# Performance work log

Hardware: AMD Instinct MI355X
Metric: run time of the kernel (lower is better)

Reference implementation:

```python
import jax, jax.numpy as jnp
import numpy as np
import math

B, L, D, H, DK, DV = 4, 1024, 1024, 16, 64, 64


def setup_inputs() -> dict:
    key0 = jax.random.key(0)
    ks = jax.random.split(key0, 12)
    s = 0.02
    return {
        "key":   jax.random.normal(ks[0], (B, L, D), jnp.float32),
        "value": jax.random.normal(ks[1], (B, L, D), jnp.float32),
        "query": jax.random.normal(ks[2], (B, L, D), jnp.float32),
        "mask":  jax.random.randint(ks[3], (B, L, L), 0, 2).astype(bool),
        "Wq": jax.random.normal(ks[4], (D, H * DK), jnp.float32) * s,
        "bq": jnp.zeros((H * DK,), jnp.float32),
        "Wk": jax.random.normal(ks[5], (D, H * DK), jnp.float32) * s,
        "bk": jnp.zeros((H * DK,), jnp.float32),
        "Wv": jax.random.normal(ks[6], (D, H * DV), jnp.float32) * s,
        "bv": jnp.zeros((H * DV,), jnp.float32),
        "Wo": jax.random.normal(ks[7], (H * DV, D), jnp.float32) * s,
        "bo": jnp.zeros((D,), jnp.float32),
    }


def _shape(x, d):
    # (B, L, H*d) -> (B, H, L, d)
    b, l, _ = x.shape
    return x.reshape(b, l, H, d).transpose(0, 2, 1, 3)


def reference(key, value, query, mask, Wq, bq, Wk, bk, Wv, bv, Wo, bo):
    k = _shape(key @ Wk + bk, DK)       # (B,H,L,DK)
    v = _shape(value @ Wv + bv, DV)     # (B,H,L,DV)
    q = _shape(query @ Wq + bq, DK) / math.sqrt(DK)
    scores = jnp.einsum("bhqd,bhkd->bhqk", q, k)  # (B,H,L,L) fp32
    scores = jnp.where(mask[:, None, :, :], jnp.float32(-1e18), scores)
    # coverage (training path, step=None): triangular cumulative penalty
    maxes = jnp.max(scores, axis=3, keepdims=True)
    exp_score = jnp.exp(scores - maxes)
    # tril-ones matmul over exp_score[:, :, :-1, :] == cumsum along query axis
    penalty_body = jnp.cumsum(exp_score[:, :, :-1, :], axis=2)
    no_penalty = jnp.ones_like(penalty_body[:, :, :1, :])
    penalty = jnp.concatenate([no_penalty, penalty_body], axis=2)
    unnorm = exp_score / (penalty + 1e-8)
    attn = unnorm / jnp.sum(unnorm, axis=3, keepdims=True)
    context = jnp.einsum("bhqk,bhkd->bhqd", attn, v)  # (B,H,L,DV)
    context = context.transpose(0, 2, 1, 3).reshape(B, L, H * DV)
    final_output = context @ Wo + bo  # (B,L,D)
    return final_output
```

## Files before the change

kernel.cpp:

```cpp
#include <hip/hip_runtime.h>
#include <hip/hip_bf16.h>


typedef unsigned short u16;
typedef unsigned int u32;
typedef __bf16 v8bf __attribute__((ext_vector_type(8)));
typedef u16    v8us __attribute__((ext_vector_type(8)));
typedef float  v4f  __attribute__((ext_vector_type(4)));

__device__ __forceinline__ u16 f2b(float f){
  __hip_bfloat16 h = __float2bfloat16(f);
  return __builtin_bit_cast(u16, h);
}

__global__ void detect_kernel(const u32* __restrict__ m, int* __restrict__ flag){
  __shared__ int sb1, sb3, snz;
  int tid = threadIdx.x;
  if (tid == 0){ sb1 = 0; sb3 = 0; snz = 0; }
  __syncthreads();
  int l1 = 0, l3 = 0, ln = 0;
  for (int i = tid; i < 65536; i += 256){
    u32 v = m[i];
    u32 b1 = (v >> 8) & 0xffu, b2 = (v >> 16) & 0xffu, b3 = (v >> 24) & 0xffu;
    l1 |= (b1 == 0x3fu);
    l3 |= (b3 == 0x3fu);
    ln |= ((b1 | b2 | b3) != 0u);
  }
  if (l1) atomicOr(&sb1, 1);
  if (l3) atomicOr(&sb3, 1);
  if (ln) atomicOr(&snz, 1);
  __syncthreads();
  if (tid == 0) *flag = sb1 ? 3 : (sb3 ? 2 : (snz ? 0 : 1));
}

__global__ __launch_bounds__(256)
void pack_mask(const void* __restrict__ m, const int* __restrict__ modep,
               u32* __restrict__ bm)
{
  const int w = blockIdx.x * 256 + threadIdx.x;
  const int mode = *modep;
  u32 out = 0;
  if (mode == 0){
    const u32* p = (const u32*)m + (size_t)w * 8;
    #pragma unroll
    for (int i = 0; i < 8; i++){
      u32 v = p[i];
      if (v & 0x000000ffu) out |= 1u << (4*i+0);
      if (v & 0x0000ff00u) out |= 1u << (4*i+1);
      if (v & 0x00ff0000u) out |= 1u << (4*i+2);
      if (v & 0xff000000u) out |= 1u << (4*i+3);
    }
  } else if (mode == 3){
    const u16* p = (const u16*)m + (size_t)w * 32;
    for (int i = 0; i < 32; i++) if (p[i]) out |= 1u << i;
  } else {
    const u32* p = (const u32*)m + (size_t)w * 32;
    for (int i = 0; i < 32; i++) if (p[i]) out |= 1u << i;
  }
  bm[w] = out;
}

__global__ __launch_bounds__(256)
void cast_bf16(const float* __restrict__ in, u16* __restrict__ out){
  const int i = blockIdx.x * 256 + threadIdx.x;
  const float4* p = (const float4*)(in + (size_t)i * 8);
  float4 a = p[0], b = p[1];
  v8us r;
  r[0]=f2b(a.x); r[1]=f2b(a.y); r[2]=f2b(a.z); r[3]=f2b(a.w);
  r[4]=f2b(b.x); r[5]=f2b(b.y); r[6]=f2b(b.z); r[7]=f2b(b.w);
  ((v8us*)out)[i] = r;
}

__global__ __launch_bounds__(256)
void transpose_cast(const float* __restrict__ W, u16* __restrict__ Wt){
  __shared__ float T[64][65];
  const int ki = blockIdx.y, ni = blockIdx.x, t = threadIdx.x;
  const int r = t >> 2, c4 = (t & 3) * 16;
  const float4* src = (const float4*)&W[(size_t)(ki*64 + r) * 1024 + ni*64 + c4];
  #pragma unroll
  for (int i = 0; i < 4; i++){
    float4 f = src[i];
    T[r][c4+4*i+0]=f.x; T[r][c4+4*i+1]=f.y; T[r][c4+4*i+2]=f.z; T[r][c4+4*i+3]=f.w;
  }
  __syncthreads();
  u16* dst = &Wt[(size_t)(ni*64 + r) * 1024 + ki*64 + c4];
  v8us o0, o1;
  #pragma unroll
  for (int j = 0; j < 8; j++){ o0[j] = f2b(T[c4+j][r]); o1[j] = f2b(T[c4+8+j][r]); }
  *(v8us*)dst = o0;
  *(v8us*)(dst + 8) = o1;
}

template<int OMODE>
__global__ __launch_bounds__(256)
void gemm_gl(const u16* __restrict__ A, const u16* __restrict__ Wt,
             const float* __restrict__ bias, float scale, void* __restrict__ outp)
{
  __shared__ alignas(16) u16 As[128 * 64];
  __shared__ alignas(16) u16 Bs[64 * 64];
  const int tid = threadIdx.x, l = tid & 63, w = tid >> 6;
  const int li = l & 15, g = l >> 4;
  const int rowBase = blockIdx.y * 128, colBase = blockIdx.x * 64;
  const int wm = w >> 1, wn = w & 1;

  v4f acc[4][2];
  #pragma unroll
  for (int i = 0; i < 4; i++)
    #pragma unroll
    for (int j = 0; j < 2; j++) acc[i][j] = (v4f){0.f,0.f,0.f,0.f};

  for (int kt = 0; kt < 16; ++kt){
    const int k0 = kt * 64;
    __syncthreads();
    #pragma unroll
    for (int j = 0; j < 4; ++j){
      const int s = j * 256 + tid;
      const int r = s >> 3, c8 = s & 7;
      const int c8s = c8 ^ (r & 7);
      const u16* src = &A[(size_t)(rowBase + r) * 1024 + k0 + c8s * 8];
      __builtin_amdgcn_global_load_lds(
        (const __attribute__((address_space(1))) void*)src,
        (__attribute__((address_space(3))) void*)(As + (size_t)(j*256 + w*64) * 8),
        16, 0, 0);
    }
    #pragma unroll
    for (int j = 0; j < 2; ++j){
      const int s = j * 256 + tid;
      const int r = s >> 3, c8 = s & 7;
      const int c8s = c8 ^ (r & 7);
      const u16* src = &Wt[(size_t)(colBase + r) * 1024 + k0 + c8s * 8];
      __builtin_amdgcn_global_load_lds(
        (const __attribute__((address_space(1))) void*)src,
        (__attribute__((address_space(3))) void*)(Bs + (size_t)(j*256 + w*64) * 8),
        16, 0, 0);
    }
    __syncthreads();
    #pragma unroll
    for (int kk = 0; kk < 2; ++kk){
      v8bf af[4], bf[2];
      #pragma unroll
      for (int mt = 0; mt < 4; ++mt){
        const int r = wm*64 + mt*16 + li;
        af[mt] = *(const v8bf*)&As[r*64 + (((kk*4 + g) ^ (r & 7)) * 8)];
      }
      #pragma unroll
      for (int nt = 0; nt < 2; ++nt){
        const int c = wn*32 + nt*16 + li;
        bf[nt] = *(const v8bf*)&Bs[c*64 + (((kk*4 + g) ^ (c & 7)) * 8)];
      }
      #pragma unroll
      for (int mt = 0; mt < 4; ++mt)
        #pragma unroll
        for (int nt = 0; nt < 2; ++nt)
          acc[mt][nt] = __builtin_amdgcn_mfma_f32_16x16x32_bf16(af[mt], bf[nt], acc[mt][nt], 0, 0, 0);
    }
  }

  #pragma unroll
  for (int mt = 0; mt < 4; ++mt){
    #pragma unroll
    for (int nt = 0; nt < 2; ++nt){
      const int gc = colBase + wn*32 + nt*16 + li;
      const float bs = bias[gc];
      #pragma unroll
      for (int r = 0; r < 4; ++r){
        const int gr = rowBase + wm*64 + mt*16 + g*4 + r;
        float v = acc[mt][nt][r] + bs;
        if (OMODE == 0){
          v *= scale;
          const int bb = gr >> 10, lp = gr & 1023;
          const int h = gc >> 6, dk = gc & 63;
          ((u16*)outp)[((((size_t)bb*16 + h) << 10) + lp) * 64 + dk] = f2b(v);
        } else {
          ((float*)outp)[(size_t)gr * 1024 + gc] = v;
        }
      }
    }
  }
}

__global__ __launch_bounds__(256)
void rowmax_kernel(const u16* __restrict__ Qb, const u16* __restrict__ Kb,
                   const u32* __restrict__ bm, float* __restrict__ mbuf)
{
  const int tid = threadIdx.x, l = tid & 63, w = tid >> 6;
  const int li = l & 15, g = l >> 4;
  const int bid = blockIdx.x;
  const int bh = bid >> 4, qb = bid & 15;
  const int b = bh >> 4;
  const int qrow0 = qb * 64 + w * 16;
  const u32* bmb = bm + ((size_t)b << 15);

  const u16* qbase = &Qb[((size_t)bh * 1024 + qrow0 + li) * 64 + g * 8];
  const v8bf a0 = *(const v8bf*)qbase;
  const v8bf a1 = *(const v8bf*)(qbase + 32);

  float rm[4] = {-3.0e38f, -3.0e38f, -3.0e38f, -3.0e38f};

  for (int kt = 0; kt < 64; ++kt){
    const u16* kbase = &Kb[((size_t)bh * 1024 + kt*16 + li) * 64 + g * 8];
    v8bf b0 = *(const v8bf*)kbase;
    v8bf b1 = *(const v8bf*)(kbase + 32);
    v4f s = (v4f){0.f,0.f,0.f,0.f};
    s = __builtin_amdgcn_mfma_f32_16x16x32_bf16(a0, b0, s, 0, 0, 0);
    s = __builtin_amdgcn_mfma_f32_16x16x32_bf16(a1, b1, s, 0, 0, 0);
    const int bit = ((kt & 1) << 4) + li;
    #pragma unroll
    for (int r = 0; r < 4; ++r){
      const int row = qrow0 + g*4 + r;
      const u32 mw = bmb[(row << 5) | (kt >> 1)];
      const float sv = ((mw >> bit) & 1u) ? -1e18f : s[r];
      rm[r] = fmaxf(rm[r], sv);
    }
  }
  #pragma unroll
  for (int r = 0; r < 4; ++r){
    float v = rm[r];
    v = fmaxf(v, __shfl_xor(v, 1));
    v = fmaxf(v, __shfl_xor(v, 2));
    v = fmaxf(v, __shfl_xor(v, 4));
    v = fmaxf(v, __shfl_xor(v, 8));
    rm[r] = v;
  }
  if (li == 0){
    #pragma unroll
    for (int r = 0; r < 4; ++r)
      mbuf[(size_t)bh * 1024 + qrow0 + g*4 + r] = rm[r];
  }
}

__global__ __launch_bounds__(256)
void colsum_kernel(const u16* __restrict__ Qb, const u16* __restrict__ Kb,
                   const u32* __restrict__ bm, const float* __restrict__ mbuf,
                   float* __restrict__ Tsum)
{
  __shared__ float Tw[4][256];
  const int tid = threadIdx.x, l = tid & 63, w = tid >> 6;
  const int li = l & 15, g = l >> 4;
  const int bid = blockIdx.x;
  const int bh = bid >> 6, qc = (bid >> 2) & 15, kb = bid & 3;
  const int b = bh >> 4;
  const int col0 = kb * 256;
  const int qrow0 = qc * 64 + w * 16;
  const u32* bmb = bm + ((size_t)b << 15);

  const u16* qbase = &Qb[((size_t)bh * 1024 + qrow0 + li) * 64 + g * 8];
  const v8bf a0 = *(const v8bf*)qbase;
  const v8bf a1 = *(const v8bf*)(qbase + 32);
  float mrow[4];
  #pragma unroll
  for (int r = 0; r < 4; ++r) mrow[r] = mbuf[(size_t)bh * 1024 + qrow0 + g*4 + r];

  #pragma unroll
  for (int nt = 0; nt < 16; ++nt){
    const u16* kbase = &Kb[((size_t)bh * 1024 + col0 + nt*16 + li) * 64 + g * 8];
    v8bf b0 = *(const v8bf*)kbase;
    v8bf b1 = *(const v8bf*)(kbase + 32);
    v4f s = (v4f){0.f,0.f,0.f,0.f};
    s = __builtin_amdgcn_mfma_f32_16x16x32_bf16(a0, b0, s, 0, 0, 0);
    s = __builtin_amdgcn_mfma_f32_16x16x32_bf16(a1, b1, s, 0, 0, 0);
    const int wi = (col0 >> 5) + (nt >> 1);
    const int bit = ((nt & 1) << 4) + li;
    float t = 0.f;
    #pragma unroll
    for (int r = 0; r < 4; ++r){
      const int row = qrow0 + g*4 + r;
      const u32 mw = bmb[(row << 5) | wi];
      const float e = ((mw >> bit) & 1u) ? 0.f : __expf(s[r] - mrow[r]);
      t += e;
    }
    t += __shfl_xor(t, 16);
    t += __shfl_xor(t, 32);
    if (g == 0) Tw[w][nt*16 + li] = t;
  }
  __syncthreads();
  const float s4 = Tw[0][tid&255] + Tw[1][tid&255] + Tw[2][tid&255] + Tw[3][tid&255];
  Tsum[(((size_t)bh * 16 + qc) << 10) + col0 + (tid & 255)] = s4;
}

__global__ __launch_bounds__(256)
void scan_kernel(const float* __restrict__ Tsum, float* __restrict__ Cscan){
  const int bid = blockIdx.x;
  const int bh = bid >> 2, cg = bid & 3;
  const int col = cg * 256 + threadIdx.x;
  float run = 0.f;
  for (int qc = 0; qc < 16; ++qc){
    const size_t idx = (((size_t)bh * 16 + qc) << 10) + col;
    Cscan[idx] = run;
    run += Tsum[idx];
  }
}

__global__ __launch_bounds__(256, 4)
void attn2_kernel(const u16* __restrict__ Qb, const u16* __restrict__ Kb,
                  const u16* __restrict__ Vb, const u32* __restrict__ bm,
                  const float* __restrict__ mbuf, const float* __restrict__ Cscan,
                  u16* __restrict__ ctxb)
{
  __shared__ alignas(16) u16 Vt[64][136];
  __shared__ alignas(16) u16 Ulds[4][16][136];
  __shared__ float Tw[4][128];

  const int tid = threadIdx.x, l = tid & 63, w = tid >> 6;
  const int li = l & 15, g = l >> 4;
  const int bid = blockIdx.x;
  const int bh = bid >> 4, qc = bid & 15;
  const int b = bh >> 4, h = bh & 15;
  const int qrow0 = qc * 64 + w * 16;
  const u32* bmb = bm + ((size_t)b << 15);

  const u16* qbase = &Qb[((size_t)bh * 1024 + qrow0 + li) * 64 + g * 8];
  const v8bf a0 = *(const v8bf*)qbase;
  const v8bf a1 = *(const v8bf*)(qbase + 32);
  float mrow[4];
  #pragma unroll
  for (int r = 0; r < 4; ++r) mrow[r] = mbuf[(size_t)bh * 1024 + qrow0 + g*4 + r];

  v4f pv[4];
  #pragma unroll
  for (int n = 0; n < 4; ++n) pv[n] = (v4f){0.f,0.f,0.f,0.f};
  float rs[4] = {0.f, 0.f, 0.f, 0.f};

  for (int kb = 0; kb < 8; ++kb){
    const int col0 = kb * 128;
    if (kb) __syncthreads();

    #pragma unroll
    for (int j = 0; j < 4; ++j){
      const int k = (tid >> 3) + j * 32;
      const int dv0 = (tid & 7) * 8;
      v8us vv = *(const v8us*)&Vb[((size_t)bh * 1024 + col0 + k) * 64 + dv0];
      #pragma unroll
      for (int i = 0; i < 8; ++i) Vt[dv0 + i][k] = vv[i];
    }

    v4f sc[8];
    float cg16[8];
    #pragma unroll
    for (int nt = 0; nt < 8; ++nt){
      const u16* kbase = &Kb[((size_t)bh * 1024 + col0 + nt*16 + li) * 64 + g * 8];
      v8bf b0 = *(const v8bf*)kbase;
      v8bf b1 = *(const v8bf*)(kbase + 32);
      v4f s = (v4f){0.f,0.f,0.f,0.f};
      s = __builtin_amdgcn_mfma_f32_16x16x32_bf16(a0, b0, s, 0, 0, 0);
      s = __builtin_amdgcn_mfma_f32_16x16x32_bf16(a1, b1, s, 0, 0, 0);
      const int wi = (col0 >> 5) + (nt >> 1);
      const int bit = ((nt & 1) << 4) + li;
      float t = 0.f;
      #pragma unroll
      for (int r = 0; r < 4; ++r){
        const int row = qrow0 + g*4 + r;
        const u32 mw = bmb[(row << 5) | wi];
        const float e = ((mw >> bit) & 1u) ? 0.f : __expf(s[r] - mrow[r]);
        s[r] = e;
        t += e;
      }
      sc[nt] = s;
      const float t1 = __shfl_up(t, 16);
      const float t2 = __shfl_up(t, 32);
      const float t3 = __shfl_up(t, 48);
      float c = 0.f;
      if (g >= 1) c += t1;
      if (g >= 2) c += t2;
      if (g >= 3) c += t3;
      cg16[nt] = c;
      if (g == 3) Tw[w][nt*16 + li] = c + t;
    }
    __syncthreads();

    #pragma unroll
    for (int nt = 0; nt < 8; ++nt){
      const int c = nt*16 + li;
      float base = Cscan[(((size_t)bh * 16 + qc) << 10) + col0 + c];
      if (w > 0) base += Tw[0][c];
      if (w > 1) base += Tw[1][c];
      if (w > 2) base += Tw[2][c];
      float run = 0.f;
      #pragma unroll
      for (int r = 0; r < 4; ++r){
        const int Rg = qrow0 + g*4 + r;
        float pen = base + cg16[nt] + run;
        if (Rg == 0) pen = 1.0f;
        const float e = sc[nt][r];
        const float u = e * __builtin_amdgcn_rcpf(pen + 1e-8f);
        run += e;
        rs[r] += u;
        Ulds[w][g*4 + r][c] = f2b(u);
      }
    }

    #pragma unroll
    for (int kk = 0; kk < 4; ++kk){
      v8bf ua = *(const v8bf*)&Ulds[w][li][g*8 + kk*32];
      #pragma unroll
      for (int n = 0; n < 4; ++n){
        v8bf vb = *(const v8bf*)&Vt[n*16 + li][g*8 + kk*32];
        pv[n] = __builtin_amdgcn_mfma_f32_16x16x32_bf16(ua, vb, pv[n], 0, 0, 0);
      }
    }
  }

  #pragma unroll
  for (int r = 0; r < 4; ++r){
    float v = rs[r];
    v += __shfl_xor(v, 1);
    v += __shfl_xor(v, 2);
    v += __shfl_xor(v, 4);
    v += __shfl_xor(v, 8);
    rs[r] = v;
  }

  #pragma unroll
  for (int n = 0; n < 4; ++n){
    #pragma unroll
    for (int r = 0; r < 4; ++r){
      const int lrow = qrow0 + g*4 + r;
      const int dv = n*16 + li;
      ctxb[(((size_t)b << 10) + lrow) * 1024 + h*64 + dv] = f2b(pv[n][r] / rs[r]);
    }
  }
}

extern "C" void kernel_launch(void* const* d_in, const int* in_sizes, int n_in,
                              void* d_out, int out_size, void* d_ws, size_t ws_size,
                              hipStream_t stream)
{
  const float* key   = (const float*)d_in[0];
  const float* value = (const float*)d_in[1];
  const float* query = (const float*)d_in[2];
  const void*  mask  = d_in[3];
  const float* Wq = (const float*)d_in[4];
  const float* bq = (const float*)d_in[5];
  const float* Wk = (const float*)d_in[6];
  const float* bk = (const float*)d_in[7];
  const float* Wv = (const float*)d_in[8];
  const float* bv = (const float*)d_in[9];
  const float* Wo = (const float*)d_in[10];
  const float* bo = (const float*)d_in[11];

  if (ws_size < (58ull << 20)) return;

  char* ws = (char*)d_ws;
  u16*   Qb    = (u16*)(ws);
  u16*   Kb    = (u16*)(ws + (8ull  << 20));
  u16*   Vb    = (u16*)(ws + (16ull << 20));
  u16*   Ac    = (u16*)(ws + (24ull << 20));
  u16*   ctxb  = (u16*)(ws + (32ull << 20));
  u16*   Wtq   = (u16*)(ws + (40ull << 20));
  u16*   Wtk   = (u16*)(ws + (42ull << 20));
  u16*   Wtv   = (u16*)(ws + (44ull << 20));
  u16*   Wto   = (u16*)(ws + (46ull << 20));
  float* mbuf  = (float*)(ws + (48ull << 20));
  u32*   bmp   = (u32*)  (ws + (48ull << 20) + (256u << 10));
  int*   flag  = (int*)  (ws + (48ull << 20) + (768u << 10));
  float* Tsum  = (float*)(ws + (49ull << 20));
  float* Cscan = (float*)(ws + (53ull << 20));

  detect_kernel<<<1, 256, 0, stream>>>((const u32*)mask, flag);
  pack_mask<<<512, 256, 0, stream>>>(mask, flag, bmp);

  dim3 tg(16, 16);
  transpose_cast<<<tg, 256, 0, stream>>>(Wq, Wtq);
  transpose_cast<<<tg, 256, 0, stream>>>(Wk, Wtk);
  transpose_cast<<<tg, 256, 0, stream>>>(Wv, Wtv);
  transpose_cast<<<tg, 256, 0, stream>>>(Wo, Wto);

  dim3 gg(16, 32);
  cast_bf16<<<2048, 256, 0, stream>>>(query, Ac);
  gemm_gl<0><<<gg, 256, 0, stream>>>(Ac, Wtq, bq, 0.125f, Qb);
  cast_bf16<<<2048, 256, 0, stream>>>(key, Ac);
  gemm_gl<0><<<gg, 256, 0, stream>>>(Ac, Wtk, bk, 1.0f, Kb);
  cast_bf16<<<2048, 256, 0, stream>>>(value, Ac);
  gemm_gl<0><<<gg, 256, 0, stream>>>(Ac, Wtv, bv, 1.0f, Vb);

  rowmax_kernel<<<1024, 256, 0, stream>>>(Qb, Kb, bmp, mbuf);
  colsum_kernel<<<4096, 256, 0, stream>>>(Qb, Kb, bmp, mbuf, Tsum);
  scan_kernel<<<256, 256, 0, stream>>>(Tsum, Cscan);
  attn2_kernel<<<1024, 256, 0, stream>>>(Qb, Kb, Vb, bmp, mbuf, Cscan, ctxb);

  gemm_gl<1><<<gg, 256, 0, stream>>>(ctxb, Wto, bo, 1.0f, d_out);
}
```

Measured before the change: 499.6 us.

## Write V transposed from projection GEMM and read it directly in attention

The V projection GEMM now writes its output transposed (per head, dv-major with the sequence index contiguous). The attention kernel then loads MFMA B operands for the PV product straight from global memory instead of staging and transposing V through shared memory each key block. This drops the LDS transpose and its scalar shared stores, and the launch-bounds occupancy hint is removed. The cost is that the GEMM epilogue now makes strided 2-byte global writes, and V operand loads in attention go to global/L2 instead of LDS.

```diff
diff --git a/kernel.cpp b/kernel.cpp
--- a/kernel.cpp
+++ b/kernel.cpp
@@ -171,6 +171,10 @@
           const int bb = gr >> 10, lp = gr & 1023;
           const int h = gc >> 6, dk = gc & 63;
           ((u16*)outp)[((((size_t)bb*16 + h) << 10) + lp) * 64 + dk] = f2b(v);
+        } else if (OMODE == 2){
+          const int bb = gr >> 10, lp = gr & 1023;
+          const int h = gc >> 6, dk = gc & 63;
+          ((u16*)outp)[((((size_t)bb*16 + h)*64 + dk) << 10) + lp] = f2b(v);
         } else {
           ((float*)outp)[(size_t)gr * 1024 + gc] = v;
         }
@@ -291,13 +295,12 @@
   }
 }
 
-__global__ __launch_bounds__(256, 4)
+__global__ __launch_bounds__(256)
 void attn2_kernel(const u16* __restrict__ Qb, const u16* __restrict__ Kb,
-                  const u16* __restrict__ Vb, const u32* __restrict__ bm,
+                  const u16* __restrict__ Vtg, const u32* __restrict__ bm,
                   const float* __restrict__ mbuf, const float* __restrict__ Cscan,
                   u16* __restrict__ ctxb)
 {
-  __shared__ alignas(16) u16 Vt[64][136];
   __shared__ alignas(16) u16 Ulds[4][16][136];
   __shared__ float Tw[4][128];
 
@@ -325,25 +328,16 @@
     const int col0 = kb * 128;
     if (kb) __syncthreads();
 
-    #pragma unroll
-    for (int j = 0; j < 4; ++j){
-      const int k = (tid >> 3) + j * 32;
-      const int dv0 = (tid & 7) * 8;
-      v8us vv = *(const v8us*)&Vb[((size_t)bh * 1024 + col0 + k) * 64 + dv0];
-      #pragma unroll
-      for (int i = 0; i < 8; ++i) Vt[dv0 + i][k] = vv[i];
-    }
-
     v4f sc[8];
     float cg16[8];
     #pragma unroll
     for (int nt = 0; nt < 8; ++nt){
       const u16* kbase = &Kb[((size_t)bh * 1024 + col0 + nt*16 + li) * 64 + g * 8];
-      v8bf b0 = *(const v8bf*)kbase;
-      v8bf b1 = *(const v8bf*)(kbase + 32);
+      v8bf b0f = *(const v8bf*)kbase;
+      v8bf b1f = *(const v8bf*)(kbase + 32);
       v4f s = (v4f){0.f,0.f,0.f,0.f};
-      s = __builtin_amdgcn_mfma_f32_16x16x32_bf16(a0, b0, s, 0, 0, 0);
-      s = __builtin_amdgcn_mfma_f32_16x16x32_bf16(a1, b1, s, 0, 0, 0);
+      s = __builtin_amdgcn_mfma_f32_16x16x32_bf16(a0, b0f, s, 0, 0, 0);
+      s = __builtin_amdgcn_mfma_f32_16x16x32_bf16(a1, b1f, s, 0, 0, 0);
       const int wi = (col0 >> 5) + (nt >> 1);
       const int bit = ((nt & 1) << 4) + li;
       float t = 0.f;
@@ -394,7 +388,7 @@
       v8bf ua = *(const v8bf*)&Ulds[w][li][g*8 + kk*32];
       #pragma unroll
       for (int n = 0; n < 4; ++n){
-        v8bf vb = *(const v8bf*)&Vt[n*16 + li][g*8 + kk*32];
+        const v8bf vb = *(const v8bf*)&Vtg[(size_t)(bh*64 + n*16 + li) * 1024 + col0 + kk*32 + g*8];
         pv[n] = __builtin_amdgcn_mfma_f32_16x16x32_bf16(ua, vb, pv[n], 0, 0, 0);
       }
     }
@@ -443,7 +437,7 @@
   char* ws = (char*)d_ws;
   u16*   Qb    = (u16*)(ws);
   u16*   Kb    = (u16*)(ws + (8ull  << 20));
-  u16*   Vb    = (u16*)(ws + (16ull << 20));
+  u16*   Vtg   = (u16*)(ws + (16ull << 20));
   u16*   Ac    = (u16*)(ws + (24ull << 20));
   u16*   ctxb  = (u16*)(ws + (32ull << 20));
   u16*   Wtq   = (u16*)(ws + (40ull << 20));
@@ -471,12 +465,12 @@
   cast_bf16<<<2048, 256, 0, stream>>>(key, Ac);
   gemm_gl<0><<<gg, 256, 0, stream>>>(Ac, Wtk, bk, 1.0f, Kb);
   cast_bf16<<<2048, 256, 0, stream>>>(value, Ac);
-  gemm_gl<0><<<gg, 256, 0, stream>>>(Ac, Wtv, bv, 1.0f, Vb);
+  gemm_gl<2><<<gg, 256, 0, stream>>>(Ac, Wtv, bv, 1.0f, Vtg);
 
   rowmax_kernel<<<1024, 256, 0, stream>>>(Qb, Kb, bmp, mbuf);
   colsum_kernel<<<4096, 256, 0, stream>>>(Qb, Kb, bmp, mbuf, Tsum);
   scan_kernel<<<256, 256, 0, stream>>>(Tsum, Cscan);
-  attn2_kernel<<<1024, 256, 0, stream>>>(Qb, Kb, Vb, bmp, mbuf, Cscan, ctxb);
+  attn2_kernel<<<1024, 256, 0, stream>>>(Qb, Kb, Vtg, bmp, mbuf, Cscan, ctxb);
 
   gemm_gl<1><<<gg, 256, 0, stream>>>(ctxb, Wto, bo, 1.0f, d_out);
 }
```

New measurement: 552.7 us. 10.6% more time.
